# Kernel tuning notes

Measured on AMD Instinct MI355X. Metric: run time of the kernel, lower is better.

Reference implementation:

```python
import jax, jax.numpy as jnp
import numpy as np

EMBED = 1024
HEADS = 16
HEAD_DIM = EMBED // HEADS
MLP_DIM = 4096
EPS = 1e-5


def setup_inputs() -> dict:
    key = jax.random.key(0)
    ks = jax.random.split(key, 12)
    s = lambda d: 1.0 / np.sqrt(d)
    return {
        "x": jax.random.normal(ks[0], (8, 1024, EMBED), dtype=jnp.float32),
        "ln1_g": jnp.ones((EMBED,), jnp.float32),
        "ln1_b": jnp.zeros((EMBED,), jnp.float32),
        "w_qkv": jax.random.normal(ks[1], (EMBED, 3 * EMBED), jnp.float32) * s(EMBED),
        "b_qkv": jnp.zeros((3 * EMBED,), jnp.float32),
        "w_proj": jax.random.normal(ks[2], (EMBED, EMBED), jnp.float32) * s(EMBED),
        "b_proj": jnp.zeros((EMBED,), jnp.float32),
        "ln2_g": jnp.ones((EMBED,), jnp.float32),
        "ln2_b": jnp.zeros((EMBED,), jnp.float32),
        "w_fc1": jax.random.normal(ks[3], (EMBED, MLP_DIM), jnp.float32) * s(EMBED),
        "b_fc1": jnp.zeros((MLP_DIM,), jnp.float32),
        "w_fc2": jax.random.normal(ks[4], (MLP_DIM, EMBED), jnp.float32) * s(MLP_DIM),
        "b_fc2": jnp.zeros((EMBED,), jnp.float32),
    }


def _layernorm(x, g, b):
    mu = jnp.mean(x, axis=-1, keepdims=True)
    var = jnp.mean(jnp.square(x - mu), axis=-1, keepdims=True)
    return (x - mu) * jax.lax.rsqrt(var + EPS) * g + b


def reference(x, ln1_g, ln1_b, w_qkv, b_qkv, w_proj, b_proj,
              ln2_g, ln2_b, w_fc1, b_fc1, w_fc2, b_fc2):
    B, N, D = x.shape
    scale = HEAD_DIM ** -0.5

    # --- attention branch ---
    h = _layernorm(x, ln1_g, ln1_b)
    qkv = h @ w_qkv + b_qkv                       # [B,N,3D]
    qkv = qkv.reshape(B, N, 3, HEADS, HEAD_DIM)
    q, k, v = jnp.moveaxis(qkv, 2, 0)             # each [B,N,H,hd]
    attn = jnp.einsum('bqhd,bkhd->bhqk', q, k) * scale
    attn = jax.nn.softmax(attn, axis=-1)
    out = jnp.einsum('bhqk,bkhd->bqhd', attn, v).reshape(B, N, D)
    x = x + (out @ w_proj + b_proj)

    # --- MLP branch ---
    h = _layernorm(x, ln2_g, ln2_b)
    h = jax.nn.gelu(h @ w_fc1 + b_fc1, approximate=False)
    x = x + (h @ w_fc2 + b_fc2)
    return x
```

## Files before the change

### kernel.cpp

```cpp
#include <hip/hip_runtime.h>
#include <cstdint>


typedef unsigned short u16;
typedef short short8 __attribute__((ext_vector_type(8)));
typedef float floatx4 __attribute__((ext_vector_type(4)));

#define GLB(p) ((const __attribute__((address_space(1))) void*)(p))
#define LDSP(p) ((__attribute__((address_space(3))) void*)(p))

__device__ __forceinline__ u16 f2bf(float f) {
    uint32_t u = __float_as_uint(f);
    u += 0x7fffu + ((u >> 16) & 1u);
    return (u16)(u >> 16);
}
__device__ __forceinline__ uint32_t pack2(float a, float b) {
    return (uint32_t)f2bf(a) | ((uint32_t)f2bf(b) << 16);
}
__device__ __forceinline__ float fast_gelu(float v) {
    float u = v * (0.7978845608f + 0.0356774081f * v * v);
    float e = __expf(2.0f * u);
    float th = 1.0f - 2.0f * __builtin_amdgcn_rcpf(e + 1.0f);
    return 0.5f * v * (1.0f + th);
}

__global__ __launch_bounds__(256) void transpose_cast_kernel(
    const float* __restrict__ W, u16* __restrict__ Wt, int K, int N)
{
    __shared__ float tile[32][33];
    int n0 = blockIdx.x * 32, k0 = blockIdx.y * 32;
    int tx = threadIdx.x, ty = threadIdx.y;
    #pragma unroll
    for (int i = 0; i < 4; ++i)
        tile[ty + i * 8][tx] = W[(size_t)(k0 + ty + i * 8) * N + n0 + tx];
    __syncthreads();
    #pragma unroll
    for (int i = 0; i < 4; ++i)
        Wt[(size_t)(n0 + ty + i * 8) * K + k0 + tx] = f2bf(tile[tx][ty + i * 8]);
}

__global__ __launch_bounds__(256) void ln_kernel(
    const float* __restrict__ x, const float* __restrict__ gw,
    const float* __restrict__ bw, u16* __restrict__ out)
{
    const int row = blockIdx.x, tid = threadIdx.x;
    float4 v = ((const float4*)(x + (size_t)row * 1024))[tid];
    float s  = v.x + v.y + v.z + v.w;
    float ss = v.x * v.x + v.y * v.y + v.z * v.z + v.w * v.w;
    #pragma unroll
    for (int off = 32; off > 0; off >>= 1) {
        s  += __shfl_down(s, off);
        ss += __shfl_down(ss, off);
    }
    __shared__ float red[8];
    if ((tid & 63) == 0) { red[tid >> 6] = s; red[4 + (tid >> 6)] = ss; }
    __syncthreads();
    float S  = red[0] + red[1] + red[2] + red[3];
    float SS = red[4] + red[5] + red[6] + red[7];
    float mu  = S * (1.0f / 1024.0f);
    float var = SS * (1.0f / 1024.0f) - mu * mu;
    float rs  = rsqrtf(var + 1e-5f);
    float4 g4 = ((const float4*)gw)[tid];
    float4 b4 = ((const float4*)bw)[tid];
    u16* o = out + (size_t)row * 1024 + tid * 4;
    o[0] = f2bf((v.x - mu) * rs * g4.x + b4.x);
    o[1] = f2bf((v.y - mu) * rs * g4.y + b4.y);
    o[2] = f2bf((v.z - mu) * rs * g4.z + b4.z);
    o[3] = f2bf((v.w - mu) * rs * g4.w + b4.w);
}

#define MODE_BF16      0
#define MODE_BF16_GELU 1
#define MODE_F32_RES   2
#define MODE_QKV       3
#define MODE_F32_ACC   4

#define G3_BUFSZ 32768
#define G3_LDS_BYTES 131072

template<int MODE>
__global__ __launch_bounds__(512, 2) void gemm3_kernel(
    const u16* __restrict__ A, const u16* __restrict__ Bt,
    const float* __restrict__ bias, const float* __restrict__ res,
    void* __restrict__ outv, u16* __restrict__ vt,
    int M, int N, int lda, int ldb, int K)
{
    extern __shared__ u16 lds[];
    const int tid = threadIdx.x;
    const int wave = tid >> 6, lane = tid & 63;
    const int lg = lane >> 4, lc = lane & 15;
    const int m0 = blockIdx.y * 256, n0 = blockIdx.x * 256;
    const int wr = wave >> 2, wc = wave & 3;

    floatx4 acc[8][4];
    #pragma unroll
    for (int i = 0; i < 8; ++i)
        #pragma unroll
        for (int j = 0; j < 4; ++j) acc[i][j] = floatx4{0.f, 0.f, 0.f, 0.f};

    const int srow = lane >> 3;
    const int schunk = (lane & 7) ^ srow;

    const u16* Agl = A  + (size_t)(m0 + wave * 32 + srow) * lda + schunk * 8;
    const u16* Bgl = Bt + (size_t)(n0 + wave * 32 + srow) * ldb + schunk * 8;
    const size_t a8 = (size_t)8 * lda, b8 = (size_t)8 * ldb;

    const int nt = K >> 6;
    auto stage = [&](int b, int kk) {
        u16* base = lds + b * G3_BUFSZ;
        #pragma unroll
        for (int j = 0; j < 4; ++j)
            __builtin_amdgcn_global_load_lds(GLB(Agl + kk + j * a8),
                                             LDSP(base + (wave * 4 + j) * 512), 16, 0, 0);
        #pragma unroll
        for (int j = 0; j < 4; ++j)
            __builtin_amdgcn_global_load_lds(GLB(Bgl + kk + j * b8),
                                             LDSP(base + 16384 + (wave * 4 + j) * 512), 16, 0, 0);
    };

    stage(0, 0);
    stage(1, 64);
    asm volatile("s_waitcnt vmcnt(8)" ::: "memory");
    __builtin_amdgcn_s_barrier();
    __builtin_amdgcn_sched_barrier(0);

    int cur = 0;
    for (int t = 0; t < nt; ++t) {
        const u16* Ab = lds + cur * G3_BUFSZ;
        const u16* Bb = Ab + 16384;
        #pragma unroll
        for (int ks = 0; ks < 2; ++ks) {
            short8 fb[4];
            #pragma unroll
            for (int nn = 0; nn < 4; ++nn)
                fb[nn] = *(const short8*)&Bb[(wc * 64 + nn * 16 + lc) * 64 +
                                             (((ks * 4 + lg) ^ (lc & 7)) * 8)];
            #pragma unroll
            for (int mh = 0; mh < 2; ++mh) {
                short8 fa[4];
                #pragma unroll
                for (int mt = 0; mt < 4; ++mt)
                    fa[mt] = *(const short8*)&Ab[(wr * 128 + mh * 64 + mt * 16 + lc) * 64 +
                                                 (((ks * 4 + lg) ^ (lc & 7)) * 8)];
                __builtin_amdgcn_s_setprio(1);
                #pragma unroll
                for (int mt = 0; mt < 4; ++mt)
                    #pragma unroll
                    for (int nn = 0; nn < 4; ++nn)
                        acc[mh * 4 + mt][nn] = __builtin_amdgcn_mfma_f32_16x16x32_bf16(
                            fa[mt], fb[nn], acc[mh * 4 + mt][nn], 0, 0, 0);
                __builtin_amdgcn_s_setprio(0);
            }
        }
        asm volatile("s_waitcnt lgkmcnt(0)" ::: "memory");
        __builtin_amdgcn_s_barrier();
        __builtin_amdgcn_sched_barrier(0);
        {
            const int tn = (t + 2 < nt) ? t + 2 : nt - 1;
            stage(cur, tn << 6);
        }
        asm volatile("s_waitcnt vmcnt(8)" ::: "memory");
        __builtin_amdgcn_s_barrier();
        __builtin_amdgcn_sched_barrier(0);
        cur ^= 1;
    }

    if (MODE == MODE_QKV && n0 >= 2048) {
        #pragma unroll
        for (int mt = 0; mt < 8; ++mt) {
            #pragma unroll
            for (int nn = 0; nn < 4; ++nn) {
                const int col = n0 + wc * 64 + nn * 16 + lc;
                const float bv = bias[col];
                const int hd = col - 2048;
                const int rowbase = m0 + wr * 128 + mt * 16 + lg * 4;
                const int b = rowbase >> 10, token = rowbase & 1023;
                float v0 = acc[mt][nn][0] + bv, v1 = acc[mt][nn][1] + bv;
                float v2 = acc[mt][nn][2] + bv, v3 = acc[mt][nn][3] + bv;
                uint2 pk = {pack2(v0, v1), pack2(v2, v3)};
                *(uint2*)&vt[((size_t)b * 1024 + hd) * 1024 + token] = pk;
            }
        }
        return;
    }
    #pragma unroll
    for (int mt = 0; mt < 8; ++mt) {
        #pragma unroll
        for (int nn = 0; nn < 4; ++nn) {
            const int col = n0 + wc * 64 + nn * 16 + lc;
            const float bv = (MODE == MODE_F32_ACC) ? 0.f : bias[col];
            #pragma unroll
            for (int r = 0; r < 4; ++r) {
                const int row = m0 + wr * 128 + mt * 16 + lg * 4 + r;
                float v = acc[mt][nn][r] + bv;
                if (MODE == MODE_BF16 || MODE == MODE_QKV) {
                    ((u16*)outv)[(size_t)row * N + col] = f2bf(v);
                } else if (MODE == MODE_BF16_GELU) {
                    ((u16*)outv)[(size_t)row * N + col] = f2bf(fast_gelu(v));
                } else {
                    ((float*)outv)[(size_t)row * N + col] = v + res[(size_t)row * N + col];
                }
            }
        }
    }
}

__global__ __launch_bounds__(256) void attn_kernel(
    const u16* __restrict__ qkv, const u16* __restrict__ vtg, u16* __restrict__ out)
{
    const int bid = blockIdx.x;
    const int g = ((bid >> 7) << 3) | (bid & 7);
    const int qt = (bid >> 3) & 15;
    const int h = g & 15, b = g >> 4;
    const int tid = threadIdx.x, wave = tid >> 6, lane = tid & 63;
    const int lg = lane >> 4, lc = lane & 15;

    __shared__ __attribute__((aligned(16))) u16 Qs[64 * 64];
    __shared__ __attribute__((aligned(16))) u16 Ks[64 * 64];
    __shared__ __attribute__((aligned(16))) u16 Vts[64 * 64];
    __shared__ __attribute__((aligned(16))) u16 Ps[64 * 64];

    const int q0 = qt * 64;
    const size_t hb = ((size_t)b * 1024) * 3072 + h * 64;
    const u16* vhead = vtg + ((size_t)b * 1024 + h * 64) * 1024;
    const int srow = lane >> 3;
    const int schunk = (lane & 7) ^ srow;

    {
        const u16* Qg = qkv + hb + (size_t)(q0 + wave * 16 + srow) * 3072 + schunk * 8;
        u16* Qw = &Qs[wave * 1024];
        __builtin_amdgcn_global_load_lds(GLB(Qg), LDSP(Qw), 16, 0, 0);
        __builtin_amdgcn_global_load_lds(GLB(Qg + (size_t)8 * 3072), LDSP(Qw + 512), 16, 0, 0);
    }
    __syncthreads();
    short8 aq[2];
    aq[0] = *(const short8*)&Qs[(wave * 16 + lc) * 64 + (((0 + lg) ^ (lc & 7)) * 8)];
    aq[1] = *(const short8*)&Qs[(wave * 16 + lc) * 64 + (((4 + lg) ^ (lc & 7)) * 8)];

    floatx4 o[4];
    #pragma unroll
    for (int dt = 0; dt < 4; ++dt) o[dt] = floatx4{0.f, 0.f, 0.f, 0.f};
    float mprev = -INFINITY, lsum = 0.f;
    const float sc = 0.125f;

    for (int kt = 0; kt < 16; ++kt) {
        __syncthreads();
        {
            const u16* Kg = qkv + hb + 1024 +
                (size_t)(kt * 64 + wave * 16 + srow) * 3072 + schunk * 8;
            u16* Kw = &Ks[wave * 1024];
            __builtin_amdgcn_global_load_lds(GLB(Kg), LDSP(Kw), 16, 0, 0);
            __builtin_amdgcn_global_load_lds(GLB(Kg + (size_t)8 * 3072), LDSP(Kw + 512), 16, 0, 0);
        }
        {
            const u16* Vg = vhead + (size_t)(wave * 16 + srow) * 1024 + kt * 64 + schunk * 8;
            u16* Vw = &Vts[wave * 1024];
            __builtin_amdgcn_global_load_lds(GLB(Vg), LDSP(Vw), 16, 0, 0);
            __builtin_amdgcn_global_load_lds(GLB(Vg + (size_t)8 * 1024), LDSP(Vw + 512), 16, 0, 0);
        }
        __syncthreads();

        floatx4 st[4];
        #pragma unroll
        for (int nt = 0; nt < 4; ++nt) st[nt] = floatx4{0.f, 0.f, 0.f, 0.f};
        #pragma unroll
        for (int ks = 0; ks < 2; ++ks)
            #pragma unroll
            for (int nt = 0; nt < 4; ++nt) {
                short8 fk = *(const short8*)&Ks[(nt * 16 + lc) * 64 +
                                                (((ks * 4 + lg) ^ (lc & 7)) * 8)];
                st[nt] = __builtin_amdgcn_mfma_f32_16x16x32_bf16(fk, aq[ks], st[nt], 0, 0, 0);
            }

        float m = st[0][0];
        #pragma unroll
        for (int nt = 0; nt < 4; ++nt)
            #pragma unroll
            for (int r = 0; r < 4; ++r) m = fmaxf(m, st[nt][r]);
        m = fmaxf(m, __shfl_xor(m, 16));
        m = fmaxf(m, __shfl_xor(m, 32));
        float mn = fmaxf(mprev, m * sc);
        float aexp = __expf(mprev - mn);
        mprev = mn;

        const int q = wave * 16 + lc;
        float rs = 0.f;
        #pragma unroll
        for (int nt = 0; nt < 4; ++nt) {
            float p0 = __expf(st[nt][0] * sc - mn);
            float p1 = __expf(st[nt][1] * sc - mn);
            float p2 = __expf(st[nt][2] * sc - mn);
            float p3 = __expf(st[nt][3] * sc - mn);
            rs += (p0 + p1) + (p2 + p3);
            const int c16 = nt * 2 + (lg >> 1);
            uint2 pk = {pack2(p0, p1), pack2(p2, p3)};
            *(uint2*)&Ps[q * 64 + ((c16 ^ (lc & 7)) * 8) + (lg & 1) * 4] = pk;
        }
        rs += __shfl_xor(rs, 16);
        rs += __shfl_xor(rs, 32);
        lsum = lsum * aexp + rs;
        #pragma unroll
        for (int dt = 0; dt < 4; ++dt)
            #pragma unroll
            for (int r = 0; r < 4; ++r) o[dt][r] *= aexp;

        #pragma unroll
        for (int ks = 0; ks < 2; ++ks) {
            short8 fp = *(const short8*)&Ps[q * 64 + (((ks * 4 + lg) ^ (lc & 7)) * 8)];
            #pragma unroll
            for (int dt = 0; dt < 4; ++dt) {
                short8 fv = *(const short8*)&Vts[(dt * 16 + lc) * 64 +
                                                 (((ks * 4 + lg) ^ (lc & 7)) * 8)];
                o[dt] = __builtin_amdgcn_mfma_f32_16x16x32_bf16(fv, fp, o[dt], 0, 0, 0);
            }
        }
    }

    const float rl = 1.0f / lsum;
    const int q = q0 + wave * 16 + lc;
    #pragma unroll
    for (int dt = 0; dt < 4; ++dt) {
        uint2 pk = {pack2(o[dt][0] * rl, o[dt][1] * rl),
                    pack2(o[dt][2] * rl, o[dt][3] * rl)};
        *(uint2*)&out[((size_t)b * 1024 + q) * 1024 + h * 64 + dt * 16 + lg * 4] = pk;
    }
}

extern "C" void kernel_launch(void* const* d_in, const int* in_sizes, int n_in,
                              void* d_out, int out_size, void* d_ws, size_t ws_size,
                              hipStream_t stream)
{
    const float* x      = (const float*)d_in[0];
    const float* ln1_g  = (const float*)d_in[1];
    const float* ln1_b  = (const float*)d_in[2];
    const float* w_qkv  = (const float*)d_in[3];
    const float* b_qkv  = (const float*)d_in[4];
    const float* w_proj = (const float*)d_in[5];
    const float* b_proj = (const float*)d_in[6];
    const float* ln2_g  = (const float*)d_in[7];
    const float* ln2_b  = (const float*)d_in[8];
    const float* w_fc1  = (const float*)d_in[9];
    const float* b_fc1  = (const float*)d_in[10];
    const float* w_fc2  = (const float*)d_in[11];
    const float* b_fc2  = (const float*)d_in[12];
    float* outp = (float*)d_out;

    char* ws = (char*)d_ws;
    size_t off = 0;
    auto alloc = [&](size_t bytes) { void* p = ws + off; off += (bytes + 255) & ~(size_t)255; return p; };
    u16*  wqkvT  = (u16*)alloc((size_t)3072 * 1024 * 2);
    u16*  wprojT = (u16*)alloc((size_t)1024 * 1024 * 2);
    u16*  wfc1T  = (u16*)alloc((size_t)4096 * 1024 * 2);
    u16*  wfc2T  = (u16*)alloc((size_t)1024 * 4096 * 2);
    u16*  hbuf   = (u16*)alloc((size_t)8192 * 1024 * 2);
    u16*  big    = (u16*)alloc((size_t)8192 * 4096 * 2);
    u16*  vtbuf  = (u16*)alloc((size_t)8 * 1024 * 1024 * 2);
    u16*  attno  = (u16*)alloc((size_t)8192 * 1024 * 2);
    float* x2    = (float*)alloc((size_t)8192 * 1024 * 4);
    float* pbuf  = (float*)vtbuf;

    static bool attr_done = []{
        hipFuncSetAttribute(reinterpret_cast<const void*>(gemm3_kernel<MODE_QKV>),
                            hipFuncAttributeMaxDynamicSharedMemorySize, G3_LDS_BYTES);
        hipFuncSetAttribute(reinterpret_cast<const void*>(gemm3_kernel<MODE_BF16_GELU>),
                            hipFuncAttributeMaxDynamicSharedMemorySize, G3_LDS_BYTES);
        hipFuncSetAttribute(reinterpret_cast<const void*>(gemm3_kernel<MODE_F32_RES>),
                            hipFuncAttributeMaxDynamicSharedMemorySize, G3_LDS_BYTES);
        hipFuncSetAttribute(reinterpret_cast<const void*>(gemm3_kernel<MODE_F32_ACC>),
                            hipFuncAttributeMaxDynamicSharedMemorySize, G3_LDS_BYTES);
        return true;
    }();
    (void)attr_done;

    dim3 tb(32, 8);
    transpose_cast_kernel<<<dim3(3072 / 32, 1024 / 32), tb, 0, stream>>>(w_qkv,  wqkvT,  1024, 3072);
    transpose_cast_kernel<<<dim3(1024 / 32, 1024 / 32), tb, 0, stream>>>(w_proj, wprojT, 1024, 1024);
    transpose_cast_kernel<<<dim3(4096 / 32, 1024 / 32), tb, 0, stream>>>(w_fc1,  wfc1T,  1024, 4096);
    transpose_cast_kernel<<<dim3(1024 / 32, 4096 / 32), tb, 0, stream>>>(w_fc2,  wfc2T,  4096, 1024);

    ln_kernel<<<8192, 256, 0, stream>>>(x, ln1_g, ln1_b, hbuf);
    gemm3_kernel<MODE_QKV><<<dim3(3072 / 256, 8192 / 256), 512, G3_LDS_BYTES, stream>>>(
        hbuf, wqkvT, b_qkv, nullptr, big, vtbuf, 8192, 3072, 1024, 1024, 1024);
    attn_kernel<<<2048, 256, 0, stream>>>(big, vtbuf, attno);
    gemm3_kernel<MODE_F32_RES><<<dim3(1024 / 256, 8192 / 256), 512, G3_LDS_BYTES, stream>>>(
        attno, wprojT, b_proj, x, x2, nullptr, 8192, 1024, 1024, 1024, 1024);
    ln_kernel<<<8192, 256, 0, stream>>>(x2, ln2_g, ln2_b, hbuf);
    gemm3_kernel<MODE_BF16_GELU><<<dim3(4096 / 256, 8192 / 256), 512, G3_LDS_BYTES, stream>>>(
        hbuf, wfc1T, b_fc1, nullptr, big, nullptr, 8192, 4096, 1024, 1024, 1024);
    gemm3_kernel<MODE_F32_RES><<<dim3(1024 / 256, 8192 / 256), 512, G3_LDS_BYTES, stream>>>(
        big, wfc2T, b_fc2, x2, pbuf, nullptr, 8192, 1024, 4096, 4096, 2048);
    gemm3_kernel<MODE_F32_ACC><<<dim3(1024 / 256, 8192 / 256), 512, G3_LDS_BYTES, stream>>>(
        big + 2048, wfc2T + 2048, nullptr, pbuf, outp, nullptr, 8192, 1024, 4096, 4096, 2048);
}
```

Baseline: 554.1 us.

## Interleave half-tile loads with MFMA quadrants and run FC2 split-K concurrently

The GEMM main loop now stages A and B in 64-row halves, one half per sub-step, interleaved with four MFMA quadrant groups per K-tile. This is an 8-phase schedule with finer-grained vmcnt gating, meant to overlap global-to-LDS traffic with compute and to shorten LDS fragment reads before each MFMA burst. The FC2 split-K pair of sequential launches becomes one launch with blockIdx.z selecting the K half. The two partial results are written to separate buffers, one reusing the QKV weight workspace, and summed by a new add2 kernel. The extra pass reads and writes fp32 partials, and the reuse of the weight buffer relies on it no longer being needed.

Result: faster. 507.1 us (-8.5%).

```diff
diff --git a/kernel.cpp b/kernel.cpp
--- a/kernel.cpp
+++ b/kernel.cpp
@@ -69,17 +69,65 @@
     o[3] = f2bf((v.w - mu) * rs * g4.w + b4.w);
 }
 
+__global__ __launch_bounds__(256) void add2_kernel(
+    const float* __restrict__ a, const float* __restrict__ b,
+    float* __restrict__ o, int n4)
+{
+    int i = blockIdx.x * 256 + threadIdx.x;
+    const int stride = gridDim.x * 256;
+    for (; i < n4; i += stride) {
+        float4 va = ((const float4*)a)[i], vb = ((const float4*)b)[i];
+        ((float4*)o)[i] = make_float4(va.x + vb.x, va.y + vb.y, va.z + vb.z, va.w + vb.w);
+    }
+}
+
 #define MODE_BF16      0
 #define MODE_BF16_GELU 1
 #define MODE_F32_RES   2
 #define MODE_QKV       3
-#define MODE_F32_ACC   4
-
-#define G3_BUFSZ 32768
-#define G3_LDS_BYTES 131072
+#define MODE_F32_SPLIT 4
+
+#define G8_BUF1 32768
+#define G8_LDS_BYTES 131072
+
+#define SB()    __builtin_amdgcn_sched_barrier(0)
+#define BARR()  do { __builtin_amdgcn_s_barrier(); SB(); } while (0)
+#define GATE4() do { asm volatile("s_waitcnt vmcnt(4)" ::: "memory"); SB(); } while (0)
+#define WL0()   do { asm volatile("s_waitcnt lgkmcnt(0)" ::: "memory"); SB(); } while (0)
+
+#define RDA(DST, BUFOFF, MH) \
+    _Pragma("unroll") \
+    for (int mt = 0; mt < 4; ++mt) \
+        _Pragma("unroll") \
+        for (int ks = 0; ks < 2; ++ks) \
+            DST[mt][ks] = *(const short8*)&lds[(BUFOFF) + \
+                (size_t)(wr * 128 + (MH) * 64 + mt * 16 + lc) * 64 + \
+                (((ks * 4 + lg) ^ (lc & 7)) * 8)];
+
+#define RDB(DST, BUFOFF, NH) \
+    _Pragma("unroll") \
+    for (int nn = 0; nn < 2; ++nn) \
+        _Pragma("unroll") \
+        for (int ks = 0; ks < 2; ++ks) \
+            DST[nn][ks] = *(const short8*)&lds[(BUFOFF) + 16384 + \
+                (size_t)(wc * 64 + (NH) * 32 + nn * 16 + lc) * 64 + \
+                (((ks * 4 + lg) ^ (lc & 7)) * 8)];
+
+#define MMAQ(MH, NH, FA, FB) \
+    __builtin_amdgcn_s_setprio(1); \
+    _Pragma("unroll") \
+    for (int ks = 0; ks < 2; ++ks) \
+        _Pragma("unroll") \
+        for (int mt = 0; mt < 4; ++mt) \
+            _Pragma("unroll") \
+            for (int nn = 0; nn < 2; ++nn) \
+                acc[(MH) * 4 + mt][(NH) * 2 + nn] = \
+                    __builtin_amdgcn_mfma_f32_16x16x32_bf16( \
+                        FA[mt][ks], FB[nn][ks], acc[(MH) * 4 + mt][(NH) * 2 + nn], 0, 0, 0); \
+    __builtin_amdgcn_s_setprio(0);
 
 template<int MODE>
-__global__ __launch_bounds__(512, 2) void gemm3_kernel(
+__global__ __launch_bounds__(512, 2) void gemm8_kernel(
     const u16* __restrict__ A, const u16* __restrict__ Bt,
     const float* __restrict__ bias, const float* __restrict__ res,
     void* __restrict__ outv, u16* __restrict__ vt,
@@ -91,6 +139,8 @@
     const int lg = lane >> 4, lc = lane & 15;
     const int m0 = blockIdx.y * 256, n0 = blockIdx.x * 256;
     const int wr = wave >> 2, wc = wave & 3;
+    const int zed = (MODE == MODE_F32_SPLIT) ? blockIdx.z : 0;
+    if (MODE == MODE_F32_SPLIT && zed) { A += K; Bt += K; }
 
     floatx4 acc[8][4];
     #pragma unroll
@@ -101,68 +151,56 @@
     const int srow = lane >> 3;
     const int schunk = (lane & 7) ^ srow;
 
-    const u16* Agl = A  + (size_t)(m0 + wave * 32 + srow) * lda + schunk * 8;
-    const u16* Bgl = Bt + (size_t)(n0 + wave * 32 + srow) * ldb + schunk * 8;
-    const size_t a8 = (size_t)8 * lda, b8 = (size_t)8 * ldb;
+    const u16* Abase = A  + (size_t)(m0 + wave * 8 + srow) * lda + schunk * 8;
+    const u16* Bbase = Bt + (size_t)(n0 + wave * 8 + srow) * ldb + schunk * 8;
+
+    auto stageH = [&](int b, int o, int h, int kk) {
+        if (o == 0) {
+            const u16* src = Abase + (size_t)h * 128 * lda + kk;
+            u16* dst = lds + b * G8_BUF1 + h * 8192 + wave * 512;
+            __builtin_amdgcn_global_load_lds(GLB(src), LDSP(dst), 16, 0, 0);
+            __builtin_amdgcn_global_load_lds(GLB(src + (size_t)64 * lda), LDSP(dst + 4096), 16, 0, 0);
+        } else {
+            const u16* src = Bbase + (size_t)h * 128 * ldb + kk;
+            u16* dst = lds + b * G8_BUF1 + 16384 + h * 8192 + wave * 512;
+            __builtin_amdgcn_global_load_lds(GLB(src), LDSP(dst), 16, 0, 0);
+            __builtin_amdgcn_global_load_lds(GLB(src + (size_t)64 * ldb), LDSP(dst + 4096), 16, 0, 0);
+        }
+    };
 
     const int nt = K >> 6;
-    auto stage = [&](int b, int kk) {
-        u16* base = lds + b * G3_BUFSZ;
-        #pragma unroll
-        for (int j = 0; j < 4; ++j)
-            __builtin_amdgcn_global_load_lds(GLB(Agl + kk + j * a8),
-                                             LDSP(base + (wave * 4 + j) * 512), 16, 0, 0);
-        #pragma unroll
-        for (int j = 0; j < 4; ++j)
-            __builtin_amdgcn_global_load_lds(GLB(Bgl + kk + j * b8),
-                                             LDSP(base + 16384 + (wave * 4 + j) * 512), 16, 0, 0);
-    };
-
-    stage(0, 0);
-    stage(1, 64);
-    asm volatile("s_waitcnt vmcnt(8)" ::: "memory");
-    __builtin_amdgcn_s_barrier();
-    __builtin_amdgcn_sched_barrier(0);
-
-    int cur = 0;
-    for (int t = 0; t < nt; ++t) {
-        const u16* Ab = lds + cur * G3_BUFSZ;
-        const u16* Bb = Ab + 16384;
-        #pragma unroll
-        for (int ks = 0; ks < 2; ++ks) {
-            short8 fb[4];
-            #pragma unroll
-            for (int nn = 0; nn < 4; ++nn)
-                fb[nn] = *(const short8*)&Bb[(wc * 64 + nn * 16 + lc) * 64 +
-                                             (((ks * 4 + lg) ^ (lc & 7)) * 8)];
-            #pragma unroll
-            for (int mh = 0; mh < 2; ++mh) {
-                short8 fa[4];
-                #pragma unroll
-                for (int mt = 0; mt < 4; ++mt)
-                    fa[mt] = *(const short8*)&Ab[(wr * 128 + mh * 64 + mt * 16 + lc) * 64 +
-                                                 (((ks * 4 + lg) ^ (lc & 7)) * 8)];
-                __builtin_amdgcn_s_setprio(1);
-                #pragma unroll
-                for (int mt = 0; mt < 4; ++mt)
-                    #pragma unroll
-                    for (int nn = 0; nn < 4; ++nn)
-                        acc[mh * 4 + mt][nn] = __builtin_amdgcn_mfma_f32_16x16x32_bf16(
-                            fa[mt], fb[nn], acc[mh * 4 + mt][nn], 0, 0, 0);
-                __builtin_amdgcn_s_setprio(0);
-            }
-        }
-        asm volatile("s_waitcnt lgkmcnt(0)" ::: "memory");
-        __builtin_amdgcn_s_barrier();
-        __builtin_amdgcn_sched_barrier(0);
-        {
-            const int tn = (t + 2 < nt) ? t + 2 : nt - 1;
-            stage(cur, tn << 6);
-        }
-        asm volatile("s_waitcnt vmcnt(8)" ::: "memory");
-        __builtin_amdgcn_s_barrier();
-        __builtin_amdgcn_sched_barrier(0);
-        cur ^= 1;
+
+    stageH(0, 0, 0, 0); stageH(0, 0, 1, 0); stageH(0, 1, 0, 0); stageH(0, 1, 1, 0);
+    stageH(1, 0, 0, 64);
+
+    short8 fa0[4][2], fa1[4][2], fb0[2][2], fb1[2][2];
+
+    for (int t0 = 0; t0 < nt; t0 += 2) {
+        const int kk1 = (t0 + 1) * 64;
+        const int kk2 = ((t0 + 2 < nt) ? t0 + 2 : nt - 1) * 64;
+        const int kk3 = ((t0 + 3 < nt) ? t0 + 3 : nt - 1) * 64;
+        stageH(1, 0, 1, kk1); GATE4(); BARR();
+        RDA(fa0, 0, 0) RDB(fb0, 0, 0) WL0();
+        MMAQ(0, 0, fa0, fb0)
+        stageH(1, 1, 0, kk1); BARR();
+        RDA(fa1, 0, 1) WL0();
+        MMAQ(1, 0, fa1, fb0)
+        stageH(1, 1, 1, kk1); BARR();
+        RDB(fb1, 0, 1) WL0();
+        MMAQ(1, 1, fa1, fb1)
+        stageH(0, 0, 0, kk2); BARR();
+        MMAQ(0, 1, fa0, fb1)
+        stageH(0, 0, 1, kk2); GATE4(); BARR();
+        RDA(fa0, G8_BUF1, 0) RDB(fb0, G8_BUF1, 0) WL0();
+        MMAQ(0, 0, fa0, fb0)
+        stageH(0, 1, 0, kk2); BARR();
+        RDA(fa1, G8_BUF1, 1) WL0();
+        MMAQ(1, 0, fa1, fb0)
+        stageH(0, 1, 1, kk2); BARR();
+        RDB(fb1, G8_BUF1, 1) WL0();
+        MMAQ(1, 1, fa1, fb1)
+        stageH(1, 0, 0, kk3); BARR();
+        MMAQ(0, 1, fa0, fb1)
     }
 
     if (MODE == MODE_QKV && n0 >= 2048) {
@@ -183,12 +221,13 @@
         }
         return;
     }
+    float* osel = (MODE == MODE_F32_SPLIT && zed) ? (float*)vt : (float*)outv;
     #pragma unroll
     for (int mt = 0; mt < 8; ++mt) {
         #pragma unroll
         for (int nn = 0; nn < 4; ++nn) {
             const int col = n0 + wc * 64 + nn * 16 + lc;
-            const float bv = (MODE == MODE_F32_ACC) ? 0.f : bias[col];
+            const float bv = (MODE == MODE_F32_SPLIT && zed) ? 0.f : bias[col];
             #pragma unroll
             for (int r = 0; r < 4; ++r) {
                 const int row = m0 + wr * 128 + mt * 16 + lg * 4 + r;
@@ -197,8 +236,10 @@
                     ((u16*)outv)[(size_t)row * N + col] = f2bf(v);
                 } else if (MODE == MODE_BF16_GELU) {
                     ((u16*)outv)[(size_t)row * N + col] = f2bf(fast_gelu(v));
+                } else if (MODE == MODE_F32_RES) {
+                    ((float*)outv)[(size_t)row * N + col] = v + res[(size_t)row * N + col];
                 } else {
-                    ((float*)outv)[(size_t)row * N + col] = v + res[(size_t)row * N + col];
+                    osel[(size_t)row * N + col] = zed ? v : (v + res[(size_t)row * N + col]);
                 }
             }
         }
@@ -351,23 +392,24 @@
     u16*  wqkvT  = (u16*)alloc((size_t)3072 * 1024 * 2);
     u16*  wprojT = (u16*)alloc((size_t)1024 * 1024 * 2);
     u16*  wfc1T  = (u16*)alloc((size_t)4096 * 1024 * 2);
+    u16*  hbuf   = (u16*)alloc((size_t)8192 * 1024 * 2);
     u16*  wfc2T  = (u16*)alloc((size_t)1024 * 4096 * 2);
-    u16*  hbuf   = (u16*)alloc((size_t)8192 * 1024 * 2);
     u16*  big    = (u16*)alloc((size_t)8192 * 4096 * 2);
     u16*  vtbuf  = (u16*)alloc((size_t)8 * 1024 * 1024 * 2);
     u16*  attno  = (u16*)alloc((size_t)8192 * 1024 * 2);
     float* x2    = (float*)alloc((size_t)8192 * 1024 * 4);
-    float* pbuf  = (float*)vtbuf;
+    float* p0    = (float*)vtbuf;
+    float* p1    = (float*)wqkvT;
 
     static bool attr_done = []{
-        hipFuncSetAttribute(reinterpret_cast<const void*>(gemm3_kernel<MODE_QKV>),
-                            hipFuncAttributeMaxDynamicSharedMemorySize, G3_LDS_BYTES);
-        hipFuncSetAttribute(reinterpret_cast<const void*>(gemm3_kernel<MODE_BF16_GELU>),
-                            hipFuncAttributeMaxDynamicSharedMemorySize, G3_LDS_BYTES);
-        hipFuncSetAttribute(reinterpret_cast<const void*>(gemm3_kernel<MODE_F32_RES>),
-                            hipFuncAttributeMaxDynamicSharedMemorySize, G3_LDS_BYTES);
-        hipFuncSetAttribute(reinterpret_cast<const void*>(gemm3_kernel<MODE_F32_ACC>),
-                            hipFuncAttributeMaxDynamicSharedMemorySize, G3_LDS_BYTES);
+        hipFuncSetAttribute(reinterpret_cast<const void*>(gemm8_kernel<MODE_QKV>),
+                            hipFuncAttributeMaxDynamicSharedMemorySize, G8_LDS_BYTES);
+        hipFuncSetAttribute(reinterpret_cast<const void*>(gemm8_kernel<MODE_BF16_GELU>),
+                            hipFuncAttributeMaxDynamicSharedMemorySize, G8_LDS_BYTES);
+        hipFuncSetAttribute(reinterpret_cast<const void*>(gemm8_kernel<MODE_F32_RES>),
+                            hipFuncAttributeMaxDynamicSharedMemorySize, G8_LDS_BYTES);
+        hipFuncSetAttribute(reinterpret_cast<const void*>(gemm8_kernel<MODE_F32_SPLIT>),
+                            hipFuncAttributeMaxDynamicSharedMemorySize, G8_LDS_BYTES);
         return true;
     }();
     (void)attr_done;
@@ -379,16 +421,15 @@
     transpose_cast_kernel<<<dim3(1024 / 32, 4096 / 32), tb, 0, stream>>>(w_fc2,  wfc2T,  4096, 1024);
 
     ln_kernel<<<8192, 256, 0, stream>>>(x, ln1_g, ln1_b, hbuf);
-    gemm3_kernel<MODE_QKV><<<dim3(3072 / 256, 8192 / 256), 512, G3_LDS_BYTES, stream>>>(
+    gemm8_kernel<MODE_QKV><<<dim3(3072 / 256, 8192 / 256), 512, G8_LDS_BYTES, stream>>>(
         hbuf, wqkvT, b_qkv, nullptr, big, vtbuf, 8192, 3072, 1024, 1024, 1024);
     attn_kernel<<<2048, 256, 0, stream>>>(big, vtbuf, attno);
-    gemm3_kernel<MODE_F32_RES><<<dim3(1024 / 256, 8192 / 256), 512, G3_LDS_BYTES, stream>>>(
+    gemm8_kernel<MODE_F32_RES><<<dim3(1024 / 256, 8192 / 256), 512, G8_LDS_BYTES, stream>>>(
         attno, wprojT, b_proj, x, x2, nullptr, 8192, 1024, 1024, 1024, 1024);
     ln_kernel<<<8192, 256, 0, stream>>>(x2, ln2_g, ln2_b, hbuf);
-    gemm3_kernel<MODE_BF16_GELU><<<dim3(4096 / 256, 8192 / 256), 512, G3_LDS_BYTES, stream>>>(
+    gemm8_kernel<MODE_BF16_GELU><<<dim3(4096 / 256, 8192 / 256), 512, G8_LDS_BYTES, stream>>>(
         hbuf, wfc1T, b_fc1, nullptr, big, nullptr, 8192, 4096, 1024, 1024, 1024);
-    gemm3_kernel<MODE_F32_RES><<<dim3(1024 / 256, 8192 / 256), 512, G3_LDS_BYTES, stream>>>(
-        big, wfc2T, b_fc2, x2, pbuf, nullptr, 8192, 1024, 4096, 4096, 2048);
-    gemm3_kernel<MODE_F32_ACC><<<dim3(1024 / 256, 8192 / 256), 512, G3_LDS_BYTES, stream>>>(
-        big + 2048, wfc2T + 2048, nullptr, pbuf, outp, nullptr, 8192, 1024, 4096, 4096, 2048);
-}
+    gemm8_kernel<MODE_F32_SPLIT><<<dim3(1024 / 256, 8192 / 256, 2), 512, G8_LDS_BYTES, stream>>>(
+        big, wfc2T, b_fc2, x2, p0, (u16*)p1, 8192, 1024, 4096, 4096, 2048);
+    add2_kernel<<<2048, 256, 0, stream>>>(p0, p1, outp, 8192 * 1024 / 4);
+}
```

## Switch GEMMs to 128x128 tiles with XCD-aware block remap, drop split-K

Applied to the files above, without the earlier changes.

Replaces the 256x256-tile, 512-thread GEMM with a 128x128-tile, 256-thread variant using half the LDS. Block indices are remapped so consecutive tiles land on the same XCD, which should improve L2 locality. The FC2 GEMM no longer splits K into two launches with an intermediate fp32 buffer and runs as one full-K launch. Smaller tiles give more blocks and better occupancy and wave balance on the smaller-N GEMMs, but each block reuses less data per LDS load.

Result: faster. 471.7 us (-14.9%).

```diff
diff --git a/kernel.cpp b/kernel.cpp
--- a/kernel.cpp
+++ b/kernel.cpp
@@ -73,13 +73,12 @@
 #define MODE_BF16_GELU 1
 #define MODE_F32_RES   2
 #define MODE_QKV       3
-#define MODE_F32_ACC   4
-
-#define G3_BUFSZ 32768
-#define G3_LDS_BYTES 131072
+
+#define G4_BUFSZ 16384
+#define G4_LDS_BYTES 65536
 
 template<int MODE>
-__global__ __launch_bounds__(512, 2) void gemm3_kernel(
+__global__ __launch_bounds__(256, 2) void gemm4_kernel(
     const u16* __restrict__ A, const u16* __restrict__ Bt,
     const float* __restrict__ bias, const float* __restrict__ res,
     void* __restrict__ outv, u16* __restrict__ vt,
@@ -89,12 +88,16 @@
     const int tid = threadIdx.x;
     const int wave = tid >> 6, lane = tid & 63;
     const int lg = lane >> 4, lc = lane & 15;
-    const int m0 = blockIdx.y * 256, n0 = blockIdx.x * 256;
-    const int wr = wave >> 2, wc = wave & 3;
-
-    floatx4 acc[8][4];
-    #pragma unroll
-    for (int i = 0; i < 8; ++i)
+    const int nx = gridDim.x, nwg = nx * gridDim.y;
+    const int orig = blockIdx.y * nx + blockIdx.x;
+    const int q = nwg >> 3, r = nwg & 7, xc = orig & 7, oo = orig >> 3;
+    const int sid = (xc < r ? xc * (q + 1) : r * (q + 1) + (xc - r) * q) + oo;
+    const int m0 = (sid / nx) * 128, n0 = (sid % nx) * 128;
+    const int wr = wave >> 1, wc = wave & 1;
+
+    floatx4 acc[4][4];
+    #pragma unroll
+    for (int i = 0; i < 4; ++i)
         #pragma unroll
         for (int j = 0; j < 4; ++j) acc[i][j] = floatx4{0.f, 0.f, 0.f, 0.f};
 
@@ -107,7 +110,7 @@
 
     const int nt = K >> 6;
     auto stage = [&](int b, int kk) {
-        u16* base = lds + b * G3_BUFSZ;
+        u16* base = lds + b * G4_BUFSZ;
         #pragma unroll
         for (int j = 0; j < 4; ++j)
             __builtin_amdgcn_global_load_lds(GLB(Agl + kk + j * a8),
@@ -115,7 +118,7 @@
         #pragma unroll
         for (int j = 0; j < 4; ++j)
             __builtin_amdgcn_global_load_lds(GLB(Bgl + kk + j * b8),
-                                             LDSP(base + 16384 + (wave * 4 + j) * 512), 16, 0, 0);
+                                             LDSP(base + 8192 + (wave * 4 + j) * 512), 16, 0, 0);
     };
 
     stage(0, 0);
@@ -126,31 +129,27 @@
 
     int cur = 0;
     for (int t = 0; t < nt; ++t) {
-        const u16* Ab = lds + cur * G3_BUFSZ;
-        const u16* Bb = Ab + 16384;
+        const u16* Ab = lds + cur * G4_BUFSZ;
+        const u16* Bb = Ab + 8192;
         #pragma unroll
         for (int ks = 0; ks < 2; ++ks) {
-            short8 fb[4];
+            short8 fa[4], fb[4];
+            #pragma unroll
+            for (int mt = 0; mt < 4; ++mt)
+                fa[mt] = *(const short8*)&Ab[(wr * 64 + mt * 16 + lc) * 64 +
+                                             (((ks * 4 + lg) ^ (lc & 7)) * 8)];
             #pragma unroll
             for (int nn = 0; nn < 4; ++nn)
                 fb[nn] = *(const short8*)&Bb[(wc * 64 + nn * 16 + lc) * 64 +
                                              (((ks * 4 + lg) ^ (lc & 7)) * 8)];
-            #pragma unroll
-            for (int mh = 0; mh < 2; ++mh) {
-                short8 fa[4];
+            __builtin_amdgcn_s_setprio(1);
+            #pragma unroll
+            for (int mt = 0; mt < 4; ++mt)
                 #pragma unroll
-                for (int mt = 0; mt < 4; ++mt)
-                    fa[mt] = *(const short8*)&Ab[(wr * 128 + mh * 64 + mt * 16 + lc) * 64 +
-                                                 (((ks * 4 + lg) ^ (lc & 7)) * 8)];
-                __builtin_amdgcn_s_setprio(1);
-                #pragma unroll
-                for (int mt = 0; mt < 4; ++mt)
-                    #pragma unroll
-                    for (int nn = 0; nn < 4; ++nn)
-                        acc[mh * 4 + mt][nn] = __builtin_amdgcn_mfma_f32_16x16x32_bf16(
-                            fa[mt], fb[nn], acc[mh * 4 + mt][nn], 0, 0, 0);
-                __builtin_amdgcn_s_setprio(0);
-            }
+                for (int nn = 0; nn < 4; ++nn)
+                    acc[mt][nn] = __builtin_amdgcn_mfma_f32_16x16x32_bf16(
+                        fa[mt], fb[nn], acc[mt][nn], 0, 0, 0);
+            __builtin_amdgcn_s_setprio(0);
         }
         asm volatile("s_waitcnt lgkmcnt(0)" ::: "memory");
         __builtin_amdgcn_s_barrier();
@@ -164,16 +163,17 @@
         __builtin_amdgcn_sched_barrier(0);
         cur ^= 1;
     }
+    asm volatile("s_waitcnt vmcnt(0)" ::: "memory");
 
     if (MODE == MODE_QKV && n0 >= 2048) {
         #pragma unroll
-        for (int mt = 0; mt < 8; ++mt) {
+        for (int mt = 0; mt < 4; ++mt) {
             #pragma unroll
             for (int nn = 0; nn < 4; ++nn) {
                 const int col = n0 + wc * 64 + nn * 16 + lc;
                 const float bv = bias[col];
                 const int hd = col - 2048;
-                const int rowbase = m0 + wr * 128 + mt * 16 + lg * 4;
+                const int rowbase = m0 + wr * 64 + mt * 16 + lg * 4;
                 const int b = rowbase >> 10, token = rowbase & 1023;
                 float v0 = acc[mt][nn][0] + bv, v1 = acc[mt][nn][1] + bv;
                 float v2 = acc[mt][nn][2] + bv, v3 = acc[mt][nn][3] + bv;
@@ -184,14 +184,14 @@
         return;
     }
     #pragma unroll
-    for (int mt = 0; mt < 8; ++mt) {
+    for (int mt = 0; mt < 4; ++mt) {
         #pragma unroll
         for (int nn = 0; nn < 4; ++nn) {
             const int col = n0 + wc * 64 + nn * 16 + lc;
-            const float bv = (MODE == MODE_F32_ACC) ? 0.f : bias[col];
+            const float bv = bias[col];
             #pragma unroll
             for (int r = 0; r < 4; ++r) {
-                const int row = m0 + wr * 128 + mt * 16 + lg * 4 + r;
+                const int row = m0 + wr * 64 + mt * 16 + lg * 4 + r;
                 float v = acc[mt][nn][r] + bv;
                 if (MODE == MODE_BF16 || MODE == MODE_QKV) {
                     ((u16*)outv)[(size_t)row * N + col] = f2bf(v);
@@ -357,17 +357,14 @@
     u16*  vtbuf  = (u16*)alloc((size_t)8 * 1024 * 1024 * 2);
     u16*  attno  = (u16*)alloc((size_t)8192 * 1024 * 2);
     float* x2    = (float*)alloc((size_t)8192 * 1024 * 4);
-    float* pbuf  = (float*)vtbuf;
 
     static bool attr_done = []{
-        hipFuncSetAttribute(reinterpret_cast<const void*>(gemm3_kernel<MODE_QKV>),
-                            hipFuncAttributeMaxDynamicSharedMemorySize, G3_LDS_BYTES);
-        hipFuncSetAttribute(reinterpret_cast<const void*>(gemm3_kernel<MODE_BF16_GELU>),
-                            hipFuncAttributeMaxDynamicSharedMemorySize, G3_LDS_BYTES);
-        hipFuncSetAttribute(reinterpret_cast<const void*>(gemm3_kernel<MODE_F32_RES>),
-                            hipFuncAttributeMaxDynamicSharedMemorySize, G3_LDS_BYTES);
-        hipFuncSetAttribute(reinterpret_cast<const void*>(gemm3_kernel<MODE_F32_ACC>),
-                            hipFuncAttributeMaxDynamicSharedMemorySize, G3_LDS_BYTES);
+        hipFuncSetAttribute(reinterpret_cast<const void*>(gemm4_kernel<MODE_QKV>),
+                            hipFuncAttributeMaxDynamicSharedMemorySize, G4_LDS_BYTES);
+        hipFuncSetAttribute(reinterpret_cast<const void*>(gemm4_kernel<MODE_BF16_GELU>),
+                            hipFuncAttributeMaxDynamicSharedMemorySize, G4_LDS_BYTES);
+        hipFuncSetAttribute(reinterpret_cast<const void*>(gemm4_kernel<MODE_F32_RES>),
+                            hipFuncAttributeMaxDynamicSharedMemorySize, G4_LDS_BYTES);
         return true;
     }();
     (void)attr_done;
@@ -379,16 +376,14 @@
     transpose_cast_kernel<<<dim3(1024 / 32, 4096 / 32), tb, 0, stream>>>(w_fc2,  wfc2T,  4096, 1024);
 
     ln_kernel<<<8192, 256, 0, stream>>>(x, ln1_g, ln1_b, hbuf);
-    gemm3_kernel<MODE_QKV><<<dim3(3072 / 256, 8192 / 256), 512, G3_LDS_BYTES, stream>>>(
+    gemm4_kernel<MODE_QKV><<<dim3(3072 / 128, 8192 / 128), 256, G4_LDS_BYTES, stream>>>(
         hbuf, wqkvT, b_qkv, nullptr, big, vtbuf, 8192, 3072, 1024, 1024, 1024);
     attn_kernel<<<2048, 256, 0, stream>>>(big, vtbuf, attno);
-    gemm3_kernel<MODE_F32_RES><<<dim3(1024 / 256, 8192 / 256), 512, G3_LDS_BYTES, stream>>>(
+    gemm4_kernel<MODE_F32_RES><<<dim3(1024 / 128, 8192 / 128), 256, G4_LDS_BYTES, stream>>>(
         attno, wprojT, b_proj, x, x2, nullptr, 8192, 1024, 1024, 1024, 1024);
     ln_kernel<<<8192, 256, 0, stream>>>(x2, ln2_g, ln2_b, hbuf);
-    gemm3_kernel<MODE_BF16_GELU><<<dim3(4096 / 256, 8192 / 256), 512, G3_LDS_BYTES, stream>>>(
+    gemm4_kernel<MODE_BF16_GELU><<<dim3(4096 / 128, 8192 / 128), 256, G4_LDS_BYTES, stream>>>(
         hbuf, wfc1T, b_fc1, nullptr, big, nullptr, 8192, 4096, 1024, 1024, 1024);
-    gemm3_kernel<MODE_F32_RES><<<dim3(1024 / 256, 8192 / 256), 512, G3_LDS_BYTES, stream>>>(
-        big, wfc2T, b_fc2, x2, pbuf, nullptr, 8192, 1024, 4096, 4096, 2048);
-    gemm3_kernel<MODE_F32_ACC><<<dim3(1024 / 256, 8192 / 256), 512, G3_LDS_BYTES, stream>>>(
-        big + 2048, wfc2T + 2048, nullptr, pbuf, outp, nullptr, 8192, 1024, 4096, 4096, 2048);
-}
+    gemm4_kernel<MODE_F32_RES><<<dim3(1024 / 128, 8192 / 128), 256, G4_LDS_BYTES, stream>>>(
+        big, wfc2T, b_fc2, x2, outp, nullptr, 8192, 1024, 4096, 4096, 4096);
+}
```
